# Kernel optimization log

Hardware: AMD Instinct MI355X
Metric: run time of the kernel (lower is better)

The kernel has to match this reference:

```python
import jax, jax.numpy as jnp
import numpy as np

D_INNER = 1024
STATE = 16
DT_RANK = 64  # ceil(d_inner / 16)
LOG_EPS = -7.0
CLAMP = 20.0


def setup_inputs() -> dict:
    key = jax.random.key(0)
    ks = jax.random.split(key, 4)
    B, L = 2, 1024
    x = jax.random.normal(ks[0], (B, L, D_INNER), jnp.float32)
    # x_proj: Linear(d_inner -> dt_rank + 2*state_size, bias=False); stored as (in, out)
    W_xproj = jax.random.normal(ks[1], (D_INNER, DT_RANK + 2 * STATE), jnp.float32) * 0.02
    # dt_proj: Linear(dt_rank -> d_inner, bias=True)
    W_dt = jax.random.normal(ks[2], (DT_RANK, D_INNER), jnp.float32) * 0.02
    b_dt = jax.random.normal(ks[3], (D_INNER,), jnp.float32) * 0.02
    # A_log = log(arange(1..state_size)) repeated over d_inner rows
    A_log = jnp.log(jnp.tile(jnp.arange(1, STATE + 1, dtype=jnp.float32), (D_INNER, 1)))
    D = jnp.ones((D_INNER,), jnp.float32)
    return {"x": x, "W_xproj": W_xproj, "W_dt": W_dt, "b_dt": b_dt, "A_log": A_log, "D": D}


def reference(x, W_xproj, W_dt, b_dt, A_log, D):
    # x: (B, L, d_inner)
    proj = x @ W_xproj  # (B, L, dt_rank + 2*N)
    dt_inter = proj[..., :DT_RANK]
    B_ssm = proj[..., DT_RANK:DT_RANK + STATE]   # (B, L, N)
    C_ssm = proj[..., DT_RANK + STATE:]          # (B, L, N)

    delta = jax.nn.softplus(dt_inter @ W_dt + b_dt)  # (B, L, d_inner)

    # discretization (ZOH)
    A = -jnp.exp(A_log)  # (d_inner, N), negative
    log_delta_A = jnp.clip(delta[..., None] * A[None, None], LOG_EPS, CLAMP)
    delta_A = jnp.exp(log_delta_A)                              # (B, L, d, N)
    delta_B_u = (delta[..., None] * B_ssm[:, :, None, :]) * x[..., None]  # (B, L, d, N)

    # log-space cumsum scan
    log_dA = jnp.log(jnp.clip(delta_A, 1e-7, None))
    log_R = jnp.cumsum(log_dA, axis=1)
    R = jnp.exp(jnp.minimum(log_R, CLAMP))
    exp_neg_log_R = jnp.exp(jnp.minimum(-log_R, CLAMP))
    S = jnp.cumsum(delta_B_u * exp_neg_log_R, axis=1)
    h = R * S  # (B, L, d, N)

    y = jnp.einsum('bln,bldn->bld', C_ssm, h) + x * D
    return y
```

## Files before the change

### kernel.cpp

```cpp
#include <hip/hip_runtime.h>
#include <math.h>

#define D_INNER 1024
#define STATE   16
#define DT_RANK 64
#define NPROJ   96
#define LSEQ    1024
#define NBATCH  2

#define LOG2E   1.4426950408889634f
#define NEG7L2  (-7.0f * LOG2E)
#define P20L2   (20.0f * LOG2E)

template<int CTRL, int RMASK>
__device__ __forceinline__ float dppadd(float v) {
    int t = __builtin_amdgcn_update_dpp(0, __float_as_int(v), CTRL, RMASK, 0xf, false);
    return v + __int_as_float(t);
}
__device__ __forceinline__ float wave_iscan(float v) {
    v = dppadd<0x111, 0xf>(v);
    v = dppadd<0x112, 0xf>(v);
    v = dppadd<0x114, 0xf>(v);
    v = dppadd<0x118, 0xf>(v);
    v = dppadd<0x142, 0xa>(v);
    v = dppadd<0x143, 0xc>(v);
    return v;
}

__global__ __launch_bounds__(768) void proj_kernel(
        const float* __restrict__ x, const float* __restrict__ Wx,
        float* __restrict__ projdt, float* __restrict__ Bg, float* __restrict__ Cg) {
    const int tid = threadIdx.x;
    const int j  = tid % 96;
    const int kq = tid / 96;
    const int row0 = blockIdx.x * 8;

    __shared__ float xs[8 * 1024];
    __shared__ float red[8][8][96];

    {
        const float4* src = (const float4*)(x + (size_t)row0 * 1024);
        #pragma unroll
        for (int i = 0; i < 3; ++i) {
            int idx = tid + 768 * i;
            if (idx < 2048) {
                float4 v = src[idx];
                *(float4*)&xs[idx * 4] = v;
            }
        }
    }
    __syncthreads();

    const float* wp = Wx + (size_t)(kq * 128) * 96 + j;
    const float* xk = &xs[kq * 128];

    float a[8];
    #pragma unroll
    for (int r = 0; r < 8; ++r) a[r] = 0.f;

    #pragma unroll 8
    for (int k = 0; k < 128; ++k) {
        float w = wp[(size_t)k * 96];
        #pragma unroll
        for (int r = 0; r < 8; ++r)
            a[r] = fmaf(xk[r * 1024 + k], w, a[r]);
    }

    #pragma unroll
    for (int r = 0; r < 8; ++r) red[kq][r][j] = a[r];
    __syncthreads();

    {
        const int r  = tid / 96;
        const int jj = tid % 96;
        float s = 0.f;
        #pragma unroll
        for (int p = 0; p < 8; ++p) s += red[p][r][jj];
        const int row = row0 + r;
        const int b = row >> 10, l = row & 1023;
        if (jj < 64)      projdt[(size_t)row * 64 + jj] = s;
        else if (jj < 80) Bg[((size_t)b * 16 + (jj - 64)) * 1024 + l] = s;
        else              Cg[((size_t)b * 16 + (jj - 80)) * 1024 + l] = s;
    }
}

__global__ __launch_bounds__(256) void delta_kernel(
        const float* __restrict__ projdt, const float* __restrict__ Wdt,
        const float* __restrict__ bdt, const float* __restrict__ x,
        float* __restrict__ delta_t, float* __restrict__ u_t) {
    const int bid = blockIdx.x;
    const int lt = bid >> 4;
    const int dt = bid & 15;
    const int row0 = lt * 64;
    const int d0 = dt * 64;
    const int tid = threadIdx.x;

    __shared__ float pl[64][69];
    __shared__ float wlbuf[64 * 68];
    __shared__ float dtile[64][65];
    float (*wl)[68] = (float(*)[68])wlbuf;

    {
        const float4* src = (const float4*)(projdt + (size_t)row0 * 64);
        #pragma unroll
        for (int i = 0; i < 4; ++i) {
            int f4i = tid + 256 * i;
            float4 v = src[f4i];
            int l = f4i >> 4, k4 = (f4i & 15) << 2;
            pl[l][k4+0] = v.x; pl[l][k4+1] = v.y; pl[l][k4+2] = v.z; pl[l][k4+3] = v.w;
        }
    }
    {
        #pragma unroll
        for (int i = 0; i < 4; ++i) {
            int f4i = tid + 256 * i;
            int k = f4i >> 4, m4 = (f4i & 15) << 2;
            float4 v = *(const float4*)(Wdt + (size_t)k * 1024 + d0 + m4);
            *(float4*)&wl[k][m4] = v;
        }
    }
    __syncthreads();

    const int lsub = tid & 63;
    const int dq = tid >> 6;
    float acc[16];
    #pragma unroll
    for (int i = 0; i < 16; ++i) acc[i] = 0.f;

    #pragma unroll 4
    for (int k = 0; k < 64; ++k) {
        float p = pl[lsub][k];
        const float4* wr = (const float4*)&wl[k][dq * 16];
        float4 w0 = wr[0], w1 = wr[1], w2 = wr[2], w3 = wr[3];
        acc[0]  = fmaf(p, w0.x, acc[0]);  acc[1]  = fmaf(p, w0.y, acc[1]);
        acc[2]  = fmaf(p, w0.z, acc[2]);  acc[3]  = fmaf(p, w0.w, acc[3]);
        acc[4]  = fmaf(p, w1.x, acc[4]);  acc[5]  = fmaf(p, w1.y, acc[5]);
        acc[6]  = fmaf(p, w1.z, acc[6]);  acc[7]  = fmaf(p, w1.w, acc[7]);
        acc[8]  = fmaf(p, w2.x, acc[8]);  acc[9]  = fmaf(p, w2.y, acc[9]);
        acc[10] = fmaf(p, w2.z, acc[10]); acc[11] = fmaf(p, w2.w, acc[11]);
        acc[12] = fmaf(p, w3.x, acc[12]); acc[13] = fmaf(p, w3.y, acc[13]);
        acc[14] = fmaf(p, w3.z, acc[14]); acc[15] = fmaf(p, w3.w, acc[15]);
    }

    #pragma unroll
    for (int i = 0; i < 16; ++i) {
        float v = acc[i] + bdt[d0 + dq * 16 + i];
        float sp = fmaxf(v, 0.f) + log1pf(__expf(-fabsf(v)));
        dtile[dq * 16 + i][lsub] = sp;
    }
    __syncthreads();

    float (*xs)[65] = (float(*)[65])wlbuf;
    {
        #pragma unroll
        for (int i = 0; i < 4; ++i) {
            int f4i = tid + 256 * i;
            int l = f4i >> 4, m4 = (f4i & 15) << 2;
            float4 v = *(const float4*)(x + (size_t)(row0 + l) * 1024 + d0 + m4);
            xs[l][m4+0] = v.x; xs[l][m4+1] = v.y; xs[l][m4+2] = v.z; xs[l][m4+3] = v.w;
        }
    }
    __syncthreads();

    {
        int dp_ = tid >> 2, seg = tid & 3;
        int b = row0 >> 10, l0 = row0 & 1023;
        size_t off = ((size_t)b * 1024 + d0 + dp_) * 1024 + l0 + seg * 16;
        float* ddst = delta_t + off;
        float* udst = u_t + off;
        #pragma unroll
        for (int m = 0; m < 4; ++m) {
            int lb = seg * 16 + m * 4;
            float4 v;
            v.x = dtile[dp_][lb + 0];
            v.y = dtile[dp_][lb + 1];
            v.z = dtile[dp_][lb + 2];
            v.w = dtile[dp_][lb + 3];
            float4 u;
            u.x = v.x * xs[lb + 0][dp_];
            u.y = v.y * xs[lb + 1][dp_];
            u.z = v.z * xs[lb + 2][dp_];
            u.w = v.w * xs[lb + 3][dp_];
            ((float4*)ddst)[m] = v;
            ((float4*)udst)[m] = u;
        }
    }
}

__global__ __launch_bounds__(256) void scan_kernel(
        float* delta_m,
        const float* __restrict__ u_t,
        const float* __restrict__ Bg, const float* __restrict__ Cg,
        const float* __restrict__ A_log, const float* __restrict__ Dvec) {
    const int bid0 = blockIdx.x;
    const int bid  = (bid0 & 7) * 64 + (bid0 >> 3);
    const int w    = threadIdx.x >> 6;
    const int lane = threadIdx.x & 63;
    const int chain = bid * 4 + w;
    const int b = chain >> 10;
    const int d = chain & 1023;
    const int l0 = lane * 16;

    const size_t choff = ((size_t)b * 1024 + d) * 1024 + l0;

    float dl[16], ul[16];
    #pragma unroll
    for (int k = 0; k < 4; ++k) {
        float4 v = *(const float4*)(delta_m + choff + k * 4);
        dl[4*k+0] = v.x; dl[4*k+1] = v.y; dl[4*k+2] = v.z; dl[4*k+3] = v.w;
    }
    #pragma unroll
    for (int k = 0; k < 4; ++k) {
        float4 v = *(const float4*)(u_t + choff + k * 4);
        ul[4*k+0] = v.x; ul[4*k+1] = v.y; ul[4*k+2] = v.z; ul[4*k+3] = v.w;
    }

    const float* Bp = Bg + (size_t)b * 16 * 1024 + l0;
    const float* Cp = Cg + (size_t)b * 16 * 1024 + l0;
    const float Dd = Dvec[d];

    float y[16];
    #pragma unroll
    for (int l = 0; l < 16; ++l)
        y[l] = ul[l] * __builtin_amdgcn_rcpf(dl[l]) * Dd;

    #pragma unroll 1
    for (int n = 0; n < 16; ++n) {
        const float a = -__expf(A_log[d * 16 + n]) * LOG2E;

        float local = 0.f;
        #pragma unroll
        for (int l = 0; l < 16; ++l)
            local += fmaxf(dl[l] * a, NEG7L2);
        float incl = wave_iscan(local);
        float c = incl - local;

        float Bv[16], Cv[16];
        #pragma unroll
        for (int k = 0; k < 4; ++k) {
            float4 bv = *(const float4*)(Bp + (size_t)n * 1024 + k * 4);
            Bv[4*k+0] = bv.x; Bv[4*k+1] = bv.y; Bv[4*k+2] = bv.z; Bv[4*k+3] = bv.w;
            float4 cv = *(const float4*)(Cp + (size_t)n * 1024 + k * 4);
            Cv[4*k+0] = cv.x; Cv[4*k+1] = cv.y; Cv[4*k+2] = cv.z; Cv[4*k+3] = cv.w;
        }

        float g[16];
        float srun = 0.f;
        #pragma unroll
        for (int l = 0; l < 16; ++l) {
            c += fmaxf(dl[l] * a, NEG7L2);
            g[l] = Cv[l] * exp2f(c);
            srun = fmaf(ul[l] * Bv[l], exp2f(fminf(-c, P20L2)), srun);
            y[l] = fmaf(g[l], srun, y[l]);
        }

        float incl2 = wave_iscan(srun);
        float lex = incl2 - srun;
        #pragma unroll
        for (int l = 0; l < 16; ++l)
            y[l] = fmaf(g[l], lex, y[l]);
    }

    #pragma unroll
    for (int k = 0; k < 4; ++k) {
        float4 o = make_float4(y[4*k+0], y[4*k+1], y[4*k+2], y[4*k+3]);
        *(float4*)(delta_m + choff + k * 4) = o;
    }
}

__global__ __launch_bounds__(256) void finish_kernel(
        const float* __restrict__ M, float* __restrict__ y) {
    const int bid = blockIdx.x;
    const int b  = bid >> 8;
    const int t  = bid & 255;
    const int tl = t >> 4;
    const int td = t & 15;
    const int tid = threadIdx.x;

    __shared__ float T[64][65];

    const float* Mb = M + (size_t)b * 1024 * 1024;
    float* yb = y + (size_t)b * 1024 * 1024;

    #pragma unroll
    for (int i = 0; i < 4; ++i) {
        int fi = tid + 256 * i;
        int r = fi >> 4, c4 = (fi & 15) << 2;
        float4 v = *(const float4*)(Mb + (size_t)(td * 64 + r) * 1024 + tl * 64 + c4);
        T[r][c4+0] = v.x; T[r][c4+1] = v.y; T[r][c4+2] = v.z; T[r][c4+3] = v.w;
    }
    __syncthreads();

    #pragma unroll
    for (int i = 0; i < 4; ++i) {
        int fi = tid + 256 * i;
        int r = fi >> 4, c4 = (fi & 15) << 2;
        float4 o;
        o.x = T[c4+0][r];
        o.y = T[c4+1][r];
        o.z = T[c4+2][r];
        o.w = T[c4+3][r];
        *(float4*)(yb + (size_t)(tl * 64 + r) * 1024 + td * 64 + c4) = o;
    }
}

extern "C" void kernel_launch(void* const* d_in, const int* in_sizes, int n_in,
                              void* d_out, int out_size, void* d_ws, size_t ws_size,
                              hipStream_t stream) {
    const float* x    = (const float*)d_in[0];
    const float* Wx   = (const float*)d_in[1];
    const float* Wdt  = (const float*)d_in[2];
    const float* bdt  = (const float*)d_in[3];
    const float* Alog = (const float*)d_in[4];
    const float* Dvec = (const float*)d_in[5];
    float* y = (float*)d_out;

    float* projdt  = (float*)d_ws;
    float* Bgp     = projdt + (size_t)2048 * 64;
    float* Cgp     = Bgp + (size_t)2 * 16 * 1024;
    float* delta_t = Cgp + (size_t)2 * 16 * 1024;
    float* u_t     = delta_t + (size_t)2 * 1024 * 1024;

    proj_kernel<<<256, 768, 0, stream>>>(x, Wx, projdt, Bgp, Cgp);
    delta_kernel<<<512, 256, 0, stream>>>(projdt, Wdt, bdt, x, delta_t, u_t);
    scan_kernel<<<512, 256, 0, stream>>>(delta_t, u_t, Bgp, Cgp, Alog, Dvec);
    finish_kernel<<<512, 256, 0, stream>>>(delta_t, y);
}
```

Before: 71.15 us.

## Fuse output transpose into scan kernel and prefetch next B/C state rows

The separate finish_kernel transpose is removed. The scan kernel now stages each block's four d-chains in padded shared memory and writes y directly in (L, d) layout using float4 stores of four adjacent d values. This avoids a full write and re-read of an intermediate 8 MB buffer and one kernel launch. In exchange the global stores are narrow 16-byte chunks strided by 4 KB. The B/C loads for the next state are also issued one iteration ahead to hide latency, which costs extra registers.

```diff
diff --git a/kernel.cpp b/kernel.cpp
--- a/kernel.cpp
+++ b/kernel.cpp
@@ -188,10 +188,10 @@
 }
 
 __global__ __launch_bounds__(256) void scan_kernel(
-        float* delta_m,
-        const float* __restrict__ u_t,
+        const float* __restrict__ delta_t, const float* __restrict__ u_t,
         const float* __restrict__ Bg, const float* __restrict__ Cg,
-        const float* __restrict__ A_log, const float* __restrict__ Dvec) {
+        const float* __restrict__ A_log, const float* __restrict__ Dvec,
+        float* __restrict__ yout) {
     const int bid0 = blockIdx.x;
     const int bid  = (bid0 & 7) * 64 + (bid0 >> 3);
     const int w    = threadIdx.x >> 6;
@@ -201,12 +201,14 @@
     const int d = chain & 1023;
     const int l0 = lane * 16;
 
+    __shared__ float T[4][1088];
+
     const size_t choff = ((size_t)b * 1024 + d) * 1024 + l0;
 
     float dl[16], ul[16];
     #pragma unroll
     for (int k = 0; k < 4; ++k) {
-        float4 v = *(const float4*)(delta_m + choff + k * 4);
+        float4 v = *(const float4*)(delta_t + choff + k * 4);
         dl[4*k+0] = v.x; dl[4*k+1] = v.y; dl[4*k+2] = v.z; dl[4*k+3] = v.w;
     }
     #pragma unroll
@@ -224,8 +226,27 @@
     for (int l = 0; l < 16; ++l)
         y[l] = ul[l] * __builtin_amdgcn_rcpf(dl[l]) * Dd;
 
+    float Bc[16], Cc[16];
+    #pragma unroll
+    for (int k = 0; k < 4; ++k) {
+        float4 bv = *(const float4*)(Bp + k * 4);
+        Bc[4*k+0] = bv.x; Bc[4*k+1] = bv.y; Bc[4*k+2] = bv.z; Bc[4*k+3] = bv.w;
+        float4 cv = *(const float4*)(Cp + k * 4);
+        Cc[4*k+0] = cv.x; Cc[4*k+1] = cv.y; Cc[4*k+2] = cv.z; Cc[4*k+3] = cv.w;
+    }
+
     #pragma unroll 1
     for (int n = 0; n < 16; ++n) {
+        const int np = (n < 15) ? n + 1 : 15;
+        float Bn[16], Cn[16];
+        #pragma unroll
+        for (int k = 0; k < 4; ++k) {
+            float4 bv = *(const float4*)(Bp + (size_t)np * 1024 + k * 4);
+            Bn[4*k+0] = bv.x; Bn[4*k+1] = bv.y; Bn[4*k+2] = bv.z; Bn[4*k+3] = bv.w;
+            float4 cv = *(const float4*)(Cp + (size_t)np * 1024 + k * 4);
+            Cn[4*k+0] = cv.x; Cn[4*k+1] = cv.y; Cn[4*k+2] = cv.z; Cn[4*k+3] = cv.w;
+        }
+
         const float a = -__expf(A_log[d * 16 + n]) * LOG2E;
 
         float local = 0.f;
@@ -235,22 +256,13 @@
         float incl = wave_iscan(local);
         float c = incl - local;
 
-        float Bv[16], Cv[16];
-        #pragma unroll
-        for (int k = 0; k < 4; ++k) {
-            float4 bv = *(const float4*)(Bp + (size_t)n * 1024 + k * 4);
-            Bv[4*k+0] = bv.x; Bv[4*k+1] = bv.y; Bv[4*k+2] = bv.z; Bv[4*k+3] = bv.w;
-            float4 cv = *(const float4*)(Cp + (size_t)n * 1024 + k * 4);
-            Cv[4*k+0] = cv.x; Cv[4*k+1] = cv.y; Cv[4*k+2] = cv.z; Cv[4*k+3] = cv.w;
-        }
-
         float g[16];
         float srun = 0.f;
         #pragma unroll
         for (int l = 0; l < 16; ++l) {
             c += fmaxf(dl[l] * a, NEG7L2);
-            g[l] = Cv[l] * exp2f(c);
-            srun = fmaf(ul[l] * Bv[l], exp2f(fminf(-c, P20L2)), srun);
+            g[l] = Cc[l] * exp2f(c);
+            srun = fmaf(ul[l] * Bc[l], exp2f(fminf(-c, P20L2)), srun);
             y[l] = fmaf(g[l], srun, y[l]);
         }
 
@@ -259,48 +271,29 @@
         #pragma unroll
         for (int l = 0; l < 16; ++l)
             y[l] = fmaf(g[l], lex, y[l]);
-    }
-
-    #pragma unroll
-    for (int k = 0; k < 4; ++k) {
-        float4 o = make_float4(y[4*k+0], y[4*k+1], y[4*k+2], y[4*k+3]);
-        *(float4*)(delta_m + choff + k * 4) = o;
-    }
-}
-
-__global__ __launch_bounds__(256) void finish_kernel(
-        const float* __restrict__ M, float* __restrict__ y) {
-    const int bid = blockIdx.x;
-    const int b  = bid >> 8;
-    const int t  = bid & 255;
-    const int tl = t >> 4;
-    const int td = t & 15;
-    const int tid = threadIdx.x;
-
-    __shared__ float T[64][65];
-
-    const float* Mb = M + (size_t)b * 1024 * 1024;
-    float* yb = y + (size_t)b * 1024 * 1024;
-
-    #pragma unroll
-    for (int i = 0; i < 4; ++i) {
-        int fi = tid + 256 * i;
-        int r = fi >> 4, c4 = (fi & 15) << 2;
-        float4 v = *(const float4*)(Mb + (size_t)(td * 64 + r) * 1024 + tl * 64 + c4);
-        T[r][c4+0] = v.x; T[r][c4+1] = v.y; T[r][c4+2] = v.z; T[r][c4+3] = v.w;
-    }
-    __syncthreads();
-
-    #pragma unroll
-    for (int i = 0; i < 4; ++i) {
-        int fi = tid + 256 * i;
-        int r = fi >> 4, c4 = (fi & 15) << 2;
-        float4 o;
-        o.x = T[c4+0][r];
-        o.y = T[c4+1][r];
-        o.z = T[c4+2][r];
-        o.w = T[c4+3][r];
-        *(float4*)(yb + (size_t)(tl * 64 + r) * 1024 + td * 64 + c4) = o;
+
+        #pragma unroll
+        for (int l = 0; l < 16; ++l) { Bc[l] = Bn[l]; Cc[l] = Cn[l]; }
+    }
+
+    #pragma unroll
+    for (int k = 0; k < 16; ++k) {
+        int l = l0 + k;
+        T[w][l + (l >> 4)] = y[k];
+    }
+    __syncthreads();
+
+    {
+        const int d0 = (bid * 4) & 1023;
+        float* yb = yout + (size_t)b * 1024 * 1024 + d0;
+        const int t = threadIdx.x;
+        #pragma unroll
+        for (int m = 0; m < 4; ++m) {
+            int l = t * 4 + m;
+            int sw = l + (l >> 4);
+            float4 o = make_float4(T[0][sw], T[1][sw], T[2][sw], T[3][sw]);
+            *(float4*)(yb + (size_t)l * 1024) = o;
+        }
     }
 }
 
@@ -323,6 +316,5 @@
 
     proj_kernel<<<256, 768, 0, stream>>>(x, Wx, projdt, Bgp, Cgp);
     delta_kernel<<<512, 256, 0, stream>>>(projdt, Wdt, bdt, x, delta_t, u_t);
-    scan_kernel<<<512, 256, 0, stream>>>(delta_t, u_t, Bgp, Cgp, Alog, Dvec);
-    finish_kernel<<<512, 256, 0, stream>>>(delta_t, y);
-}
+    scan_kernel<<<512, 256, 0, stream>>>(delta_t, u_t, Bgp, Cgp, Alog, Dvec, y);
+}
```

Result: no change. 71.51 us (+0.5%).
